# Optimization experiments

Measured on AMD Instinct MI355X. Metric: run time of the kernel, lower is better.

The kernel has to match this reference:

```python
import jax, jax.numpy as jnp
import numpy as np


def log_g(x):
    # log of g(x) = where(x>=0, x+0.5, sigmoid(x))
    return jnp.where(x >= 0, jnp.log(jnp.maximum(x, 0) + 0.5), -jax.nn.softplus(-x))


def setup_inputs() -> dict:
    key = jax.random.key(0)
    ks = jax.random.split(key, 6)
    B, S, D, H = 4, 4096, 1024, 1024
    x = jax.random.normal(ks[0], (B, S, D), dtype=jnp.float32)
    h0 = jax.random.normal(ks[1], (B, 1, H), dtype=jnp.float32)
    # Linear params (scaled like trained weights to keep activations tame)
    Wz = jax.random.normal(ks[2], (H, D), dtype=jnp.float32) * 0.02
    bz = jax.random.normal(ks[3], (H,), dtype=jnp.float32) * 0.02
    Wh = jax.random.normal(ks[4], (H, D), dtype=jnp.float32) * 0.02
    bh = jax.random.normal(ks[5], (H,), dtype=jnp.float32) * 0.02
    return {"x": x, "h0": h0, "Wz": Wz, "bz": bz, "Wh": Wh, "bh": bh}


def reference(x, h0, Wz, bz, Wh, bh):
    # x: [B,S,D], h0: [B,1,H]
    k = jnp.einsum('bsd,hd->bsh', x, Wz) + bz            # linear_z(x)
    log_z = -jax.nn.softplus(-k)                          # log sigmoid(k)
    log_coeffs = -jax.nn.softplus(k)                      # log (1 - sigmoid(k))
    log_h0 = log_g(h0)                                    # [B,1,H]
    log_tilde_h = log_g(jnp.einsum('bsd,hd->bsh', x, Wh) + bh)
    log_coeffs = jnp.pad(log_coeffs, ((0, 0), (1, 0), (0, 0)))  # prepend zero coeff
    log_values = jnp.concatenate([log_h0, log_z + log_tilde_h], axis=1)  # [B,S+1,H]
    # parallel scan in log space
    a_star = jnp.cumsum(log_coeffs, axis=1)
    log_h = a_star + jax.lax.cumlogsumexp(log_values - a_star, axis=1)
    h = jnp.exp(log_h)
    out = h[:, 1:]                                        # last seq_len steps
    return (out, out[:, -1:])
```

## Files before the change

### kernel.cpp

```cpp
#include <hip/hip_runtime.h>
#include <stdint.h>

typedef __attribute__((ext_vector_type(4))) float f32x4;
typedef __attribute__((ext_vector_type(8))) short bf16x8;
typedef __attribute__((ext_vector_type(4))) unsigned short u16x4;
typedef __attribute__((ext_vector_type(4))) unsigned int u32x4;

constexpr int cB = 4, cS = 4096, cD = 1024, cH = 1024;
constexpr int cM = cB * cS;
constexpr int cK = cD;
constexpr int NCH = 64;
constexpr int CLEN = cS / NCH;

__device__ __forceinline__ unsigned short f2bf(float f) {
  union { float f; uint32_t u; } v; v.f = f;
  uint32_t r = v.u + 0x7FFFu + ((v.u >> 16) & 1u);
  return (unsigned short)(r >> 16);
}
__device__ __forceinline__ float bf2f(unsigned short h) {
  union { float f; uint32_t u; } v; v.u = ((uint32_t)h) << 16;
  return v.f;
}

__global__ void round_kernel(const float* __restrict__ src,
                             unsigned short* __restrict__ hi) {
  int i = (blockIdx.x * blockDim.x + threadIdx.x) * 4;
  f32x4 x = *(const f32x4*)(src + i);
  u16x4 h;
#pragma unroll
  for (int j = 0; j < 4; ++j) h[j] = f2bf(x[j]);
  *(u16x4*)(hi + i) = h;
}

constexpr int BM = 128, BN = 128, BK = 64;

__global__ __launch_bounds__(256, 2) void gemm_kernel(
    const unsigned short* __restrict__ xh,
    const unsigned short* __restrict__ wwh,
    const float* __restrict__ bz, const float* __restrict__ bhv,
    unsigned int* __restrict__ cgbuf,
    float* __restrict__ Pb, float* __restrict__ Qb)
{
  __shared__ unsigned short Ah[BM * BK], Bz[BN * BK], Bh[BN * BK];
  const int tid  = threadIdx.x;
  const int lane = tid & 63;
  const int wv   = tid >> 6;
  const int wr   = wv >> 1, wc = wv & 1;

  const int bid = blockIdx.x;
  const int xcd = bid & 7;
  const int idx = bid >> 3;
  const int mt  = xcd * 16 + (idx >> 3);
  const int nt  = idx & 7;
  const int m0 = mt * BM, n0 = nt * BN;
  const int fr = lane & 15, fq = lane >> 4;

  f32x4 accz[4][4] = {};
  f32x4 acch[4][4] = {};

  const int srow = tid >> 3;
  const int scol = (((tid & 7) ^ (srow & 7)) << 3);

  const unsigned short* gA = xh  + (size_t)m0 * cK;
  const unsigned short* gZ = wwh + (size_t)n0 * cK;
  const unsigned short* gH = wwh + (size_t)(cH + n0) * cK;

  for (int kt = 0; kt < cK / BK; ++kt) {
    const int k0 = kt * BK;
    __syncthreads();
#pragma unroll
    for (int r = 0; r < 4; ++r) {
      const int row = r * 32 + srow;
      const int ldsoff = r * 4096 + tid * 16;
      const size_t goff = (size_t)row * cK + k0 + scol;
      __builtin_amdgcn_global_load_lds((const __attribute__((address_space(1))) void*)(gA + goff),
        (__attribute__((address_space(3))) void*)((char*)Ah + ldsoff), 16, 0, 0);
      __builtin_amdgcn_global_load_lds((const __attribute__((address_space(1))) void*)(gZ + goff),
        (__attribute__((address_space(3))) void*)((char*)Bz + ldsoff), 16, 0, 0);
      __builtin_amdgcn_global_load_lds((const __attribute__((address_space(1))) void*)(gH + goff),
        (__attribute__((address_space(3))) void*)((char*)Bh + ldsoff), 16, 0, 0);
    }
    __syncthreads();
#pragma unroll
    for (int kk = 0; kk < BK / 32; ++kk) {
      bf16x8 fa[4], fz[4], fh[4];
#pragma unroll
      for (int i = 0; i < 4; ++i) {
        const int ar = wr * 64 + i * 16 + fr;
        const int ca = (kk * 64 + fq * 16) ^ ((ar & 7) << 4);
        fa[i] = *(const bf16x8*)((const char*)Ah + ar * 128 + ca);
        const int br = wc * 64 + i * 16 + fr;
        const int cb = (kk * 64 + fq * 16) ^ ((br & 7) << 4);
        fz[i] = *(const bf16x8*)((const char*)Bz + br * 128 + cb);
        fh[i] = *(const bf16x8*)((const char*)Bh + br * 128 + cb);
      }
#pragma unroll
      for (int i = 0; i < 4; ++i)
#pragma unroll
        for (int j = 0; j < 4; ++j) {
          accz[i][j] = __builtin_amdgcn_mfma_f32_16x16x32_bf16(fa[i], fz[j], accz[i][j], 0, 0, 0);
          acch[i][j] = __builtin_amdgcn_mfma_f32_16x16x32_bf16(fa[i], fh[j], acch[i][j], 0, 0, 0);
        }
    }
  }

  const int b  = mt >> 5;
  const int ch = (mt & 31) * 2 + wr;
#pragma unroll
  for (int j = 0; j < 4; ++j) {
    const int n = n0 + wc * 64 + j * 16 + fr;
    const float bz_n = bz[n];
    const float bh_n = bhv[n];
    float psg[4], qsg[4];
#pragma unroll
    for (int i = 0; i < 4; ++i) {
      float p = 1.0f, q = 0.0f;
#pragma unroll
      for (int rg = 0; rg < 4; ++rg) {
        const int m = m0 + wr * 64 + i * 16 + fq * 4 + rg;
        const float kv = accz[i][j][rg] + bz_n;
        const float av = acch[i][j][rg] + bh_n;
        const float c = 1.0f / (1.0f + expf(kv));
        const float g = (av >= 0.0f) ? (av + 0.5f) : (1.0f / (1.0f + expf(-av)));
        cgbuf[(size_t)m * cH + n] = ((uint32_t)f2bf(g) << 16) | (uint32_t)f2bf(c);
        q = c * q + (1.0f - c) * g;
        p = c * p;
      }
      float pp = __shfl_xor(p, 16), qq = __shfl_xor(q, 16);
      if (fq & 1) { q = q + p * qq; } else { q = qq + pp * q; }
      p = p * pp;
      pp = __shfl_xor(p, 32); qq = __shfl_xor(q, 32);
      if (fq & 2) { q = q + p * qq; } else { q = qq + pp * q; }
      p = p * pp;
      psg[i] = p; qsg[i] = q;
    }
    float P = psg[0], Q = qsg[0];
#pragma unroll
    for (int i = 1; i < 4; ++i) { Q = qsg[i] + psg[i] * Q; P = psg[i] * P; }
    if (fq == 0) {
      const size_t o = ((size_t)b * NCH + ch) * cH + n;
      Pb[o] = P; Qb[o] = Q;
    }
  }
}

__global__ void scan_prefix_kernel(const float* __restrict__ h0,
                                   const float* __restrict__ Pb, const float* __restrict__ Qb,
                                   float* __restrict__ hin) {
  const int wid  = (blockIdx.x * blockDim.x + threadIdx.x) >> 6;
  const int lane = threadIdx.x & 63;
  const int b = wid >> 10, h = wid & 1023;
  const size_t o = ((size_t)b * NCH + lane) * cH + h;
  float P = Pb[o], Q = Qb[o];
#pragma unroll
  for (int off = 1; off < 64; off <<= 1) {
    float Po = __shfl_up(P, off), Qo = __shfl_up(Q, off);
    if (lane >= off) { Q = P * Qo + Q; P = P * Po; }
  }
  float Pe = __shfl_up(P, 1), Qe = __shfl_up(Q, 1);
  if (lane == 0) { Pe = 1.0f; Qe = 0.0f; }
  const float x = h0[b * cH + h];
  const float h0g = (x >= 0.0f) ? (x + 0.5f) : (1.0f / (1.0f + expf(-x)));
  hin[o] = Pe * h0g + Qe;
}

__global__ void scan_write_kernel(const unsigned int* __restrict__ cg,
                                  const float* __restrict__ hin, float* __restrict__ out) {
  const int bc = blockIdx.x;
  const int b = bc / NCH, ch = bc % NCH;
  const int h4 = threadIdx.x * 4;
  f32x4 hc = *(const f32x4*)(hin + ((size_t)b * NCH + ch) * cH + h4);
  size_t base = ((size_t)b * cS + (size_t)ch * CLEN) * cH + h4;
#pragma unroll 4
  for (int i = 0; i < CLEN; ++i) {
    u32x4 v = *(const u32x4*)(cg + base + (size_t)i * cH);
#pragma unroll
    for (int j = 0; j < 4; ++j) {
      const float c = bf2f((unsigned short)(v[j] & 0xFFFFu));
      const float g = bf2f((unsigned short)(v[j] >> 16));
      hc[j] = c * hc[j] + (1.0f - c) * g;
    }
    *(f32x4*)(out + base + (size_t)i * cH) = hc;
  }
  if (ch == NCH - 1) {
    *(f32x4*)(out + (size_t)cM * cH + (size_t)b * cH + h4) = hc;
  }
}

extern "C" void kernel_launch(void* const* d_in, const int* in_sizes, int n_in,
                              void* d_out, int out_size, void* d_ws, size_t ws_size,
                              hipStream_t stream) {
  const float* x   = (const float*)d_in[0];
  const float* h0  = (const float*)d_in[1];
  const float* Wz  = (const float*)d_in[2];
  const float* bz  = (const float*)d_in[3];
  const float* Wh  = (const float*)d_in[4];
  const float* bh  = (const float*)d_in[5];

  char* ws = (char*)d_ws;
  unsigned short* xh   = (unsigned short*)(ws);
  unsigned short* wwh  = (unsigned short*)(ws + (((size_t)32) << 20));
  unsigned int*   cgbuf= (unsigned int*)(ws + (((size_t)40) << 20));
  float* Pb   = (float*)(ws + (((size_t)104) << 20));
  float* Qb   = (float*)(ws + (((size_t)105) << 20));
  float* hin  = (float*)(ws + (((size_t)106) << 20));
  float* out  = (float*)d_out;

  round_kernel<<<cM * cK / 1024, 256, 0, stream>>>(x, xh);
  round_kernel<<<cH * cK / 1024, 256, 0, stream>>>(Wz, wwh);
  round_kernel<<<cH * cK / 1024, 256, 0, stream>>>(Wh, wwh + (size_t)cH * cK);
  gemm_kernel<<<(cM / BM) * (cH / BN), 256, 0, stream>>>(xh, wwh, bz, bh, cgbuf, Pb, Qb);
  scan_prefix_kernel<<<cB * cH * 64 / 256, 256, 0, stream>>>(h0, Pb, Qb, hin);
  scan_write_kernel<<<cB * NCH, 256, 0, stream>>>(cgbuf, hin, out);
}
```

Baseline: 141.1 us.

## Double-buffer GEMM LDS tiles with BK=32 to overlap loads and MFMA

Replaces the single-buffered BK=64 load/compute loop with a two-stage double buffer at BK=32. The next tile is prefetched into LDS via global_load_lds while MFMAs run on the current tile, using a raw s_waitcnt and s_barrier per iteration. The LDS swizzle changes to fit the 64-byte rows. This halves work per barrier and doubles the barrier count, and correctness depends on the hand-written waitcnt and barrier ordering.

```diff
diff --git a/kernel.cpp b/kernel.cpp
--- a/kernel.cpp
+++ b/kernel.cpp
@@ -32,7 +32,20 @@
   *(u16x4*)(hi + i) = h;
 }
 
-constexpr int BM = 128, BN = 128, BK = 64;
+constexpr int BM = 128, BN = 128, BK = 32;
+constexpr int NT = cK / BK;
+
+#define BARRIER() asm volatile("s_barrier" ::: "memory")
+#define WAITVM0() asm volatile("s_waitcnt vmcnt(0)" ::: "memory")
+
+__device__ __forceinline__ void stage64x32(const unsigned short* __restrict__ g,
+                                           unsigned short* lds, int tid) {
+  const int row  = tid >> 2;
+  const int scol = ((tid & 3) * 8) ^ (((row >> 1) & 3) << 3);
+  __builtin_amdgcn_global_load_lds(
+      (const __attribute__((address_space(1))) void*)(g + (size_t)row * cK + scol),
+      (__attribute__((address_space(3))) void*)(lds + (size_t)tid * 8), 16, 0, 0);
+}
 
 __global__ __launch_bounds__(256, 2) void gemm_kernel(
     const unsigned short* __restrict__ xh,
@@ -41,7 +54,9 @@
     unsigned int* __restrict__ cgbuf,
     float* __restrict__ Pb, float* __restrict__ Qb)
 {
-  __shared__ unsigned short Ah[BM * BK], Bz[BN * BK], Bh[BN * BK];
+  __shared__ unsigned short Ab[2][BM * BK];
+  __shared__ unsigned short Bz[2][BN * BK];
+  __shared__ unsigned short Bh[2][BN * BK];
   const int tid  = threadIdx.x;
   const int lane = tid & 63;
   const int wv   = tid >> 6;
@@ -58,50 +73,51 @@
   f32x4 accz[4][4] = {};
   f32x4 acch[4][4] = {};
 
-  const int srow = tid >> 3;
-  const int scol = (((tid & 7) ^ (srow & 7)) << 3);
-
   const unsigned short* gA = xh  + (size_t)m0 * cK;
   const unsigned short* gZ = wwh + (size_t)n0 * cK;
   const unsigned short* gH = wwh + (size_t)(cH + n0) * cK;
 
-  for (int kt = 0; kt < cK / BK; ++kt) {
-    const int k0 = kt * BK;
-    __syncthreads();
-#pragma unroll
-    for (int r = 0; r < 4; ++r) {
-      const int row = r * 32 + srow;
-      const int ldsoff = r * 4096 + tid * 16;
-      const size_t goff = (size_t)row * cK + k0 + scol;
-      __builtin_amdgcn_global_load_lds((const __attribute__((address_space(1))) void*)(gA + goff),
-        (__attribute__((address_space(3))) void*)((char*)Ah + ldsoff), 16, 0, 0);
-      __builtin_amdgcn_global_load_lds((const __attribute__((address_space(1))) void*)(gZ + goff),
-        (__attribute__((address_space(3))) void*)((char*)Bz + ldsoff), 16, 0, 0);
-      __builtin_amdgcn_global_load_lds((const __attribute__((address_space(1))) void*)(gH + goff),
-        (__attribute__((address_space(3))) void*)((char*)Bh + ldsoff), 16, 0, 0);
-    }
-    __syncthreads();
-#pragma unroll
-    for (int kk = 0; kk < BK / 32; ++kk) {
-      bf16x8 fa[4], fz[4], fh[4];
-#pragma unroll
-      for (int i = 0; i < 4; ++i) {
-        const int ar = wr * 64 + i * 16 + fr;
-        const int ca = (kk * 64 + fq * 16) ^ ((ar & 7) << 4);
-        fa[i] = *(const bf16x8*)((const char*)Ah + ar * 128 + ca);
-        const int br = wc * 64 + i * 16 + fr;
-        const int cb = (kk * 64 + fq * 16) ^ ((br & 7) << 4);
-        fz[i] = *(const bf16x8*)((const char*)Bz + br * 128 + cb);
-        fh[i] = *(const bf16x8*)((const char*)Bh + br * 128 + cb);
+  stage64x32(gA, Ab[0], tid);
+  stage64x32(gA + (size_t)64 * cK, Ab[0] + 2048, tid);
+  stage64x32(gZ, Bz[0], tid);
+  stage64x32(gZ + (size_t)64 * cK, Bz[0] + 2048, tid);
+  stage64x32(gH, Bh[0], tid);
+  stage64x32(gH + (size_t)64 * cK, Bh[0] + 2048, tid);
+  WAITVM0();
+  BARRIER();
+
+#pragma unroll 2
+  for (int t = 0; t < NT; ++t) {
+    const int cur = t & 1, nxt = cur ^ 1;
+    const int kn = (t + 1) * BK;
+    if (t + 1 < NT) {
+      stage64x32(gA + kn, Ab[nxt], tid);
+      stage64x32(gA + (size_t)64 * cK + kn, Ab[nxt] + 2048, tid);
+      stage64x32(gZ + kn, Bz[nxt], tid);
+      stage64x32(gZ + (size_t)64 * cK + kn, Bz[nxt] + 2048, tid);
+      stage64x32(gH + kn, Bh[nxt], tid);
+      stage64x32(gH + (size_t)64 * cK + kn, Bh[nxt] + 2048, tid);
+    }
+    bf16x8 fa[4], fz[4], fh[4];
+#pragma unroll
+    for (int i = 0; i < 4; ++i) {
+      const int ar = wr * 64 + i * 16 + fr;
+      const int ca = (fq * 8) ^ (((ar >> 1) & 3) << 3);
+      fa[i] = *(const bf16x8*)(Ab[cur] + ar * 32 + ca);
+      const int br = wc * 64 + i * 16 + fr;
+      const int cb = (fq * 8) ^ (((br >> 1) & 3) << 3);
+      fz[i] = *(const bf16x8*)(Bz[cur] + br * 32 + cb);
+      fh[i] = *(const bf16x8*)(Bh[cur] + br * 32 + cb);
+    }
+#pragma unroll
+    for (int i = 0; i < 4; ++i)
+#pragma unroll
+      for (int j = 0; j < 4; ++j) {
+        accz[i][j] = __builtin_amdgcn_mfma_f32_16x16x32_bf16(fa[i], fz[j], accz[i][j], 0, 0, 0);
+        acch[i][j] = __builtin_amdgcn_mfma_f32_16x16x32_bf16(fa[i], fh[j], acch[i][j], 0, 0, 0);
       }
-#pragma unroll
-      for (int i = 0; i < 4; ++i)
-#pragma unroll
-        for (int j = 0; j < 4; ++j) {
-          accz[i][j] = __builtin_amdgcn_mfma_f32_16x16x32_bf16(fa[i], fz[j], accz[i][j], 0, 0, 0);
-          acch[i][j] = __builtin_amdgcn_mfma_f32_16x16x32_bf16(fa[i], fh[j], acch[i][j], 0, 0, 0);
-        }
-    }
+    WAITVM0();
+    BARRIER();
   }
 
   const int b  = mt >> 5;
```

Measured after the change: 154.5 us. 9.5% more time.
